# Performance work log

Measured on AMD Instinct MI355X. Metric: run time of the kernel, lower is better.

The kernel has to match this reference:

```python
import jax, jax.numpy as jnp
import numpy as np

N, D, K = 8192, 128, 30  # num_nodes, isize, k


def setup_inputs() -> dict:
    key = jax.random.key(0)
    k1, k2, k3 = jax.random.split(key, 3)
    features = jax.random.normal(k1, (N, D), dtype=jnp.float32)
    # module initializes layers to identity; perturb slightly so weights matter
    eye = jnp.eye(D, dtype=jnp.float32)
    W1 = eye + 0.02 * jax.random.normal(k2, (D, D), dtype=jnp.float32)
    W2 = eye + 0.02 * jax.random.normal(k3, (D, D), dtype=jnp.float32)
    b1 = jnp.zeros((D,), dtype=jnp.float32)
    b2 = jnp.zeros((D,), dtype=jnp.float32)
    return {"features": features, "W1": W1, "b1": b1, "W2": W2, "b2": b2, "kp1": K + 1}


def reference(features, W1, b1, W2, b2, kp1):
    # internal_forward: Linear -> ReLU -> Linear (act='relu', last layer no act)
    h = jax.nn.relu(features @ W1.T + b1)
    emb = h @ W2.T + b2
    # F.normalize(dim=1, p=2)
    emb = emb / jnp.clip(jnp.linalg.norm(emb, axis=1, keepdims=True), 1e-12, None)
    # cal_similarity_graph: dense cosine similarity [N, N]
    sim = emb @ emb.T
    # top_k: keep top (k+1) entries per row, zero the rest
    _, idx = jax.lax.top_k(sim, kp1)  # idx: [N, kp1]
    mask = jnp.zeros_like(sim).at[jnp.arange(sim.shape[0])[:, None], idx].set(1.0)
    sparse_graph = sim * mask
    # apply_non_linearity('relu', i): elementwise relu
    return jax.nn.relu(sparse_graph)
```

## Files before the change

### kernel.cpp

```cpp
#include <hip/hip_runtime.h>
#include <hip/hip_fp16.h>

#define NN 8192
#define DDIM 128
#define DELTA 0.010f
#define MAXC 256
#define SIMSTRIDE 16384

typedef short short8 __attribute__((ext_vector_type(8)));
typedef unsigned short ushort8 __attribute__((ext_vector_type(8)));
typedef float f32x16 __attribute__((ext_vector_type(16)));

__device__ __forceinline__ ushort bf16_rne(float v) {
    const unsigned x = __float_as_uint(v);
    return (ushort)((x + 0x7FFFu + ((x >> 16) & 1u)) >> 16);
}

__global__ __launch_bounds__(128, 1)
void mlp_norm_kernel(const float* __restrict__ X, const float* __restrict__ W1,
                     const float* __restrict__ b1, const float* __restrict__ W2,
                     const float* __restrict__ b2, float* __restrict__ emb,
                     ushort* __restrict__ ebh, int rowsPerBlock)
{
    const int t = threadIdx.x;
    float4 w1r[32], w2r[32];
#pragma unroll
    for (int i = 0; i < 32; ++i) w1r[i] = *(const float4*)&W1[t * DDIM + i * 4];
#pragma unroll
    for (int i = 0; i < 32; ++i) w2r[i] = *(const float4*)&W2[t * DDIM + i * 4];
    const float bb1 = b1[t], bb2 = b2[t];

    __shared__ float sx[DDIM];
    __shared__ float sh[DDIM];
    __shared__ float wred[2];

    const int row0 = blockIdx.x * rowsPerBlock;
    for (int r = 0; r < rowsPerBlock; ++r) {
        const int row = row0 + r;
        sx[t] = X[(size_t)row * DDIM + t];
        __syncthreads();
        float acc = bb1;
#pragma unroll
        for (int i = 0; i < 32; ++i) {
            const float4 xv = *(const float4*)&sx[i * 4];
            acc = fmaf(xv.x, w1r[i].x, acc);
            acc = fmaf(xv.y, w1r[i].y, acc);
            acc = fmaf(xv.z, w1r[i].z, acc);
            acc = fmaf(xv.w, w1r[i].w, acc);
        }
        sh[t] = fmaxf(acc, 0.f);
        __syncthreads();
        float acc2 = bb2;
#pragma unroll
        for (int i = 0; i < 32; ++i) {
            const float4 hv = *(const float4*)&sh[i * 4];
            acc2 = fmaf(hv.x, w2r[i].x, acc2);
            acc2 = fmaf(hv.y, w2r[i].y, acc2);
            acc2 = fmaf(hv.z, w2r[i].z, acc2);
            acc2 = fmaf(hv.w, w2r[i].w, acc2);
        }
        float sq = acc2 * acc2;
#pragma unroll
        for (int off = 1; off < 64; off <<= 1) sq += __shfl_xor(sq, off);
        if ((t & 63) == 0) wred[t >> 6] = sq;
        __syncthreads();
        const float ss = wred[0] + wred[1];
        const float inv = 1.0f / fmaxf(sqrtf(ss), 1e-12f);
        const float v = acc2 * inv;
        emb[(size_t)row * DDIM + t] = v;
        ebh[(size_t)row * DDIM + t] = bf16_rne(v);
        __syncthreads();
    }
}

__global__ __launch_bounds__(256)
void simgemm_bf16(const ushort* __restrict__ ebh, ushort* __restrict__ sim)
{
    __shared__ ushort lA[128 * 128];
    __shared__ ushort lB[128 * 128];

    const int tid = threadIdx.x;
    const int bi = blockIdx.x & 63, bj = blockIdx.x >> 6;
    const int m0 = bi << 7, n0 = bj << 7;
    const int lane = tid & 63, wid = tid >> 6;
    const int wr = wid >> 1, wc = wid & 1;
    const int frow = lane & 31, fsel = lane >> 5;

    const int srow0 = tid >> 4, sg = tid & 15;
#pragma unroll
    for (int i = 0; i < 8; ++i) {
        const int row = srow0 + i * 16;
        const int so = row * 128 + ((sg ^ (row & 15)) << 3);
        *(uint4*)&lA[so] = *(const uint4*)&ebh[(size_t)(m0 + row) * DDIM + sg * 8];
        *(uint4*)&lB[so] = *(const uint4*)&ebh[(size_t)(n0 + row) * DDIM + sg * 8];
    }
    __syncthreads();

    f32x16 acc[2][2];
#pragma unroll
    for (int mb = 0; mb < 2; ++mb)
#pragma unroll
        for (int nb = 0; nb < 2; ++nb)
#pragma unroll
            for (int q = 0; q < 16; ++q) acc[mb][nb][q] = 0.f;

#pragma unroll
    for (int ks = 0; ks < 8; ++ks) {
        const int g = ks * 2 + fsel;
        short8 av[2], bv[2];
#pragma unroll
        for (int mb = 0; mb < 2; ++mb) {
            const int r = wr * 64 + mb * 32 + frow;
            av[mb] = *(const short8*)&lA[r * 128 + ((g ^ (r & 15)) << 3)];
        }
#pragma unroll
        for (int nb = 0; nb < 2; ++nb) {
            const int r = wc * 64 + nb * 32 + frow;
            bv[nb] = *(const short8*)&lB[r * 128 + ((g ^ (r & 15)) << 3)];
        }
#pragma unroll
        for (int mb = 0; mb < 2; ++mb)
#pragma unroll
            for (int nb = 0; nb < 2; ++nb)
                acc[mb][nb] = __builtin_amdgcn_mfma_f32_32x32x16_bf16(
                    av[mb], bv[nb], acc[mb][nb], 0, 0, 0);
    }

#pragma unroll
    for (int mb = 0; mb < 2; ++mb)
#pragma unroll
        for (int nb = 0; nb < 2; ++nb)
#pragma unroll
            for (int q = 0; q < 16; ++q) {
                const int rl = (q & 3) + 8 * (q >> 2) + 4 * fsel;
                const int grow = m0 + wr * 64 + mb * 32 + rl;
                const int gcol = n0 + wc * 64 + nb * 32 + (lane & 31);
                sim[(size_t)grow * SIMSTRIDE + gcol] =
                    __half_as_ushort(__float2half_rn(acc[mb][nb][q]));
            }
}

__global__ __launch_bounds__(256)
void topk_relu_kernel(float* __restrict__ out, const float* __restrict__ emb,
                      const int* __restrict__ kp1p)
{
    const int row = blockIdx.x;
    const int t = threadIdx.x;
    const int w = t >> 6;
    const unsigned kp1 = (unsigned)kp1p[0];
    const ushort* simrow = (const ushort*)out + (size_t)row * SIMSTRIDE;
    float* rowp = out + (size_t)row * NN;

    __shared__ unsigned bitmap[NN / 32];
    __shared__ float semb[DDIM];
    __shared__ unsigned wsum[2][4];
    __shared__ unsigned wmin[4];
    __shared__ int cidx[MAXC];
    __shared__ float cval[MAXC];
    __shared__ int cnum;

    bitmap[t] = 0;
    if (t == 0) cnum = 0;
    if (t < DDIM) semb[t] = emb[(size_t)row * DDIM + t];

    unsigned u[32];
#pragma unroll
    for (int i = 0; i < 4; ++i) {
        const ushort8 v8 = *(const ushort8*)&simrow[i * 2048 + t * 8];
#pragma unroll
        for (int j = 0; j < 8; ++j)
            u[i * 8 + j] = (v8[j] < 0x8000u) ? (unsigned)v8[j] : 0u;
    }

    unsigned thr = 0, teff = 0;
    bool done = false;
    for (int b = 13; b >= 0; --b) {
        const unsigned cand = thr | (1u << b);
        unsigned cnt = 0;
#pragma unroll
        for (int i = 0; i < 32; ++i)
            cnt += (unsigned)__popcll(__ballot(u[i] >= cand));
        if ((t & 63) == 0) wsum[b & 1][w] = cnt;
        __syncthreads();
        const unsigned tot = wsum[b & 1][0] + wsum[b & 1][1] +
                             wsum[b & 1][2] + wsum[b & 1][3];
        if (tot >= kp1) {
            thr = cand;
            if (tot == kp1) {
                unsigned m = 0xFFFFFFFFu;
#pragma unroll
                for (int i = 0; i < 32; ++i)
                    if (u[i] >= cand && u[i] < m) m = u[i];
#pragma unroll
                for (int off = 1; off < 64; off <<= 1) {
                    const unsigned o = __shfl_xor(m, off);
                    if (o < m) m = o;
                }
                if ((t & 63) == 0) wmin[w] = m;
                __syncthreads();
                unsigned mm = wmin[0];
                if (wmin[1] < mm) mm = wmin[1];
                if (wmin[2] < mm) mm = wmin[2];
                if (wmin[3] < mm) mm = wmin[3];
                teff = mm;
                done = true;
                break;
            }
        }
    }
    if (!done) teff = thr;
    __syncthreads();

    unsigned hi16, lo16;
    if (thr != 0u) {
        const float Treal = __half2float(__ushort_as_half((ushort)teff));
        hi16 = (unsigned)__half_as_ushort(__float2half_rn(Treal + DELTA)) + 1u;
        const float loR = Treal - DELTA;
        if (loR <= 0.f) lo16 = 1u;
        else {
            const unsigned l = __half_as_ushort(__float2half_rn(loR));
            lo16 = (l > 1u) ? l - 1u : 1u;
        }

        unsigned acnt = 0;
#pragma unroll
        for (int q = 0; q < 32; ++q) {
            const unsigned uu = u[q];
            if (uu > hi16) ++acnt;
            else if (uu >= lo16) {
                const int p = atomicAdd(&cnum, 1);
                if (p < MAXC) cidx[p] = (q >> 3) * 2048 + t * 8 + (q & 7);
            }
        }
#pragma unroll
        for (int off = 1; off < 64; off <<= 1) acnt += __shfl_xor(acnt, off);
        if ((t & 63) == 0) wsum[0][w] = acnt;
        __syncthreads();
        const unsigned A = wsum[0][0] + wsum[0][1] + wsum[0][2] + wsum[0][3];
        const int nc = cnum < MAXC ? cnum : MAXC;

        if (t < nc) {
            const float* rb = emb + (size_t)cidx[t] * DDIM;
            float a = 0.f;
#pragma unroll 8
            for (int k = 0; k < DDIM; ++k) a = fmaf(semb[k], rb[k], a);
            cval[t] = a;
        }
        __syncthreads();
        if (t < nc) {
            const float e = cval[t];
            const int my = cidx[t];
            int r = 0;
            for (int d = 0; d < nc; ++d)
                r += (cval[d] > e) || (cval[d] == e && cidx[d] < my);
            if (A + (unsigned)r < kp1)
                atomicOr(&bitmap[my >> 5], 1u << (my & 31));
        }
        __syncthreads();
    } else {
        hi16 = 0u;
        lo16 = 0xFFFFu;
        __syncthreads();
    }

#pragma unroll
    for (int i = 0; i < 4; ++i) {
        const int col0 = i * 2048 + t * 8;
        float o[8];
#pragma unroll
        for (int j = 0; j < 8; ++j) {
            const unsigned uu = u[i * 8 + j];
            const int idx = col0 + j;
            const bool keep = (uu > hi16) ||
                              (uu >= lo16 &&
                               ((bitmap[idx >> 5] >> (idx & 31)) & 1u));
            o[j] = keep ? __half2float(__ushort_as_half((ushort)uu)) : 0.f;
        }
        *(float4*)&rowp[col0]     = make_float4(o[0], o[1], o[2], o[3]);
        *(float4*)&rowp[col0 + 4] = make_float4(o[4], o[5], o[6], o[7]);
    }
}

extern "C" void kernel_launch(void* const* d_in, const int* in_sizes, int n_in,
                              void* d_out, int out_size, void* d_ws, size_t ws_size,
                              hipStream_t stream)
{
    const float* X  = (const float*)d_in[0];
    const float* W1 = (const float*)d_in[1];
    const float* b1 = (const float*)d_in[2];
    const float* W2 = (const float*)d_in[3];
    const float* b2 = (const float*)d_in[4];
    const int* kp1  = (const int*)d_in[5];
    float* out = (float*)d_out;
    float* emb  = (float*)d_ws;
    ushort* ebh = (ushort*)((char*)d_ws + (size_t)NN * DDIM * 4);

    mlp_norm_kernel<<<512, 128, 0, stream>>>(X, W1, b1, W2, b2, emb, ebh, 16);
    simgemm_bf16<<<4096, 256, 0, stream>>>(ebh, (ushort*)out);
    topk_relu_kernel<<<NN, 256, 0, stream>>>(out, emb, kp1);
}
```

Before: 218.7 us.

## Replace bitwise radix threshold search with two-level histogram selection in top-k

The top-k threshold is now found with a two-pass shared-memory histogram: a 256-bin coarse histogram on the high bits of the fp16 similarity, a suffix scan to locate the bin holding the k-th value, then a 64-bin fine histogram inside that bin. This replaces a 14-step bitwise radix search that needed a ballot/popcount over 32 registers and a block barrier at every step. The new path adds shared-memory atomics, which can contend heavily because most values fall into a few bins. It also removes the early-exit case where the exact count was hit.

```diff
diff --git a/kernel.cpp b/kernel.cpp
--- a/kernel.cpp
+++ b/kernel.cpp
@@ -147,72 +147,82 @@
     const int row = blockIdx.x;
     const int t = threadIdx.x;
     const int w = t >> 6;
+    const int lane = t & 63;
     const unsigned kp1 = (unsigned)kp1p[0];
     const ushort* simrow = (const ushort*)out + (size_t)row * SIMSTRIDE;
     float* rowp = out + (size_t)row * NN;
 
     __shared__ unsigned bitmap[NN / 32];
     __shared__ float semb[DDIM];
-    __shared__ unsigned wsum[2][4];
-    __shared__ unsigned wmin[4];
+    __shared__ unsigned hist[4][256];
+    __shared__ unsigned h2[64];
+    __shared__ unsigned wpart[4];
+    __shared__ unsigned sBA[4];
     __shared__ int cidx[MAXC];
     __shared__ float cval[MAXC];
     __shared__ int cnum;
 
     bitmap[t] = 0;
+    hist[0][t] = 0; hist[1][t] = 0; hist[2][t] = 0; hist[3][t] = 0;
+    if (t < 64) h2[t] = 0;
+    if (t < 4) sBA[t] = 0;
     if (t == 0) cnum = 0;
     if (t < DDIM) semb[t] = emb[(size_t)row * DDIM + t];
+    __syncthreads();
 
     unsigned u[32];
 #pragma unroll
     for (int i = 0; i < 4; ++i) {
         const ushort8 v8 = *(const ushort8*)&simrow[i * 2048 + t * 8];
 #pragma unroll
-        for (int j = 0; j < 8; ++j)
-            u[i * 8 + j] = (v8[j] < 0x8000u) ? (unsigned)v8[j] : 0u;
-    }
-
-    unsigned thr = 0, teff = 0;
-    bool done = false;
-    for (int b = 13; b >= 0; --b) {
-        const unsigned cand = thr | (1u << b);
-        unsigned cnt = 0;
-#pragma unroll
-        for (int i = 0; i < 32; ++i)
-            cnt += (unsigned)__popcll(__ballot(u[i] >= cand));
-        if ((t & 63) == 0) wsum[b & 1][w] = cnt;
-        __syncthreads();
-        const unsigned tot = wsum[b & 1][0] + wsum[b & 1][1] +
-                             wsum[b & 1][2] + wsum[b & 1][3];
-        if (tot >= kp1) {
-            thr = cand;
-            if (tot == kp1) {
-                unsigned m = 0xFFFFFFFFu;
-#pragma unroll
-                for (int i = 0; i < 32; ++i)
-                    if (u[i] >= cand && u[i] < m) m = u[i];
-#pragma unroll
-                for (int off = 1; off < 64; off <<= 1) {
-                    const unsigned o = __shfl_xor(m, off);
-                    if (o < m) m = o;
-                }
-                if ((t & 63) == 0) wmin[w] = m;
-                __syncthreads();
-                unsigned mm = wmin[0];
-                if (wmin[1] < mm) mm = wmin[1];
-                if (wmin[2] < mm) mm = wmin[2];
-                if (wmin[3] < mm) mm = wmin[3];
-                teff = mm;
-                done = true;
-                break;
+        for (int j = 0; j < 8; ++j) {
+            const unsigned uu = (v8[j] < 0x8000u) ? (unsigned)v8[j] : 0u;
+            u[i * 8 + j] = uu;
+            if (uu) atomicAdd(&hist[w][uu >> 6], 1u);
+        }
+    }
+    __syncthreads();
+
+    const unsigned tot = hist[0][t] + hist[1][t] + hist[2][t] + hist[3][t];
+    unsigned s = tot;
+#pragma unroll
+    for (int off = 1; off < 64; off <<= 1) {
+        const unsigned o = __shfl_down(s, off);
+        if (lane + off < 64) s += o;
+    }
+    if (lane == 0) wpart[w] = s;
+    __syncthreads();
+    unsigned addhi = 0;
+    for (int w2 = w + 1; w2 < 4; ++w2) addhi += wpart[w2];
+    const unsigned S = s + addhi;
+    if (S >= kp1 && S - tot < kp1) { sBA[0] = (unsigned)t; sBA[1] = S - tot; }
+    if (t == 0 && wpart[0] + wpart[1] + wpart[2] + wpart[3] < kp1) sBA[3] = 1u;
+    __syncthreads();
+
+    const bool keepall = (sBA[3] != 0u);
+    if (!keepall) {
+        const unsigned binB = sBA[0];
+#pragma unroll
+        for (int q = 0; q < 32; ++q)
+            if (u[q] && (u[q] >> 6) == binB) atomicAdd(&h2[u[q] & 63u], 1u);
+        __syncthreads();
+        if (t < 64) {
+            const unsigned need = kp1 - sBA[1];
+            const unsigned h = h2[t];
+            unsigned s2 = h;
+#pragma unroll
+            for (int off = 1; off < 64; off <<= 1) {
+                const unsigned o = __shfl_down(s2, off);
+                if (t + off < 64) s2 += o;
             }
-        }
-    }
-    if (!done) teff = thr;
-    __syncthreads();
+            if (s2 >= need && s2 - h < need) sBA[2] = (binB << 6) | (unsigned)t;
+        }
+        __syncthreads();
+    }
 
     unsigned hi16, lo16;
-    if (thr != 0u) {
+    if (!keepall) {
+        const unsigned teff = sBA[2];
         const float Treal = __half2float(__ushort_as_half((ushort)teff));
         hi16 = (unsigned)__half_as_ushort(__float2half_rn(Treal + DELTA)) + 1u;
         const float loR = Treal - DELTA;
@@ -234,9 +244,9 @@
         }
 #pragma unroll
         for (int off = 1; off < 64; off <<= 1) acnt += __shfl_xor(acnt, off);
-        if ((t & 63) == 0) wsum[0][w] = acnt;
-        __syncthreads();
-        const unsigned A = wsum[0][0] + wsum[0][1] + wsum[0][2] + wsum[0][3];
+        if (lane == 0) wpart[w] = acnt;
+        __syncthreads();
+        const unsigned A = wpart[0] + wpart[1] + wpart[2] + wpart[3];
         const int nc = cnum < MAXC ? cnum : MAXC;
 
         if (t < nc) {
```

New measurement: 202.7 us. 1.08x faster.
